# Kernel optimization log

Measured on AMD Instinct MI355X. Metric: run time of the kernel, lower is better.

The kernel has to match this reference:

```python
import jax, jax.numpy as jnp
import numpy as np

B, C, N = 16, 256, 2048
DA = C // 4
BN_EPS = 1e-5


def setup_inputs() -> dict:
    key = jax.random.key(0)
    ks = jax.random.split(key, 7)
    s = lambda fan_in: 1.0 / np.sqrt(fan_in)
    return {
        "x": jax.random.normal(ks[0], (B, C, N), dtype=jnp.float32),
        "Wq": jax.random.normal(ks[1], (DA, C), dtype=jnp.float32) * s(C),
        "Wk": jax.random.normal(ks[2], (DA, C), dtype=jnp.float32) * s(C),
        "Wv": jax.random.normal(ks[3], (C, C), dtype=jnp.float32) * s(C),
        "Wp": jax.random.normal(ks[4], (C, C), dtype=jnp.float32) * s(C),
        "gamma": jnp.ones((C,), dtype=jnp.float32),
        "beta": jnp.zeros((C,), dtype=jnp.float32),
    }


def reference(x, Wq, Wk, Wv, Wp, gamma, beta):
    # 1x1 conv projections (pointwise over N)
    q = jnp.einsum("dc,bcn->bnd", Wq, x)          # [B, N, da]
    k = jnp.einsum("dc,bcm->bdm", Wk, x)          # [B, da, N]
    v = jnp.einsum("oc,bcm->bmo", Wv, x)          # [B, N, C]

    energy = jnp.einsum("bnd,bdm->bnm", q, k)     # [B, N, N]
    # offset-attention double normalization: softmax over query axis (dim=1),
    # then L1 renormalization over key axis (dim=-1)
    attn = jax.nn.softmax(energy, axis=1)
    attn = attn / (1e-9 + attn.sum(axis=-1, keepdims=True))

    fsa = jnp.einsum("bnm,bmo->bon", attn, v)     # [B, C, N]

    # proj: Conv1d(1x1, no bias) -> BatchNorm1d (training-mode batch stats) -> ReLU
    y = x - fsa
    h = jnp.einsum("oc,bcn->bon", Wp, y)          # [B, C, N]
    mean = h.mean(axis=(0, 2), keepdims=True)
    var = h.var(axis=(0, 2), keepdims=True)       # biased variance
    h = (h - mean) * jax.lax.rsqrt(var + BN_EPS)
    h = h * gamma[None, :, None] + beta[None, :, None]
    h = jax.nn.relu(h)
    return h + x
```

## Files before the change

kernel.cpp:

```cpp
#include <hip/hip_runtime.h>
#include <math.h>

#define B_ 16
#define C_ 256
#define N_ 2048
#define D_ 64
#define NP_ 2080

typedef __attribute__((ext_vector_type(8))) short bf8;
typedef __attribute__((ext_vector_type(4))) float f4;

#define MFMA16(A, Bv, Cv) __builtin_amdgcn_mfma_f32_16x16x32_bf16(A, Bv, Cv, 0, 0, 0)

__device__ __forceinline__ short f2b(float f) {
  unsigned u = __float_as_uint(f);
  u = (u + 0x7fff + ((u >> 16) & 1)) >> 16;
  return (short)u;
}
__device__ __forceinline__ float b2f(short s) {
  return __uint_as_float(((unsigned)(unsigned short)s) << 16);
}

static constexpr size_t OFF_XT = 0;
static constexpr size_t OFF_QN = (size_t)16 << 20;
static constexpr size_t OFF_KN = (size_t)20 << 20;
static constexpr size_t OFF_VT = (size_t)24 << 20;
static constexpr size_t OFF_CI = (size_t)42 << 20;
static constexpr size_t OFF_WQ = OFF_CI + ((size_t)128 << 10);
static constexpr size_t OFF_WK = OFF_WQ + ((size_t)32 << 10);
static constexpr size_t OFF_WV = OFF_WK + ((size_t)32 << 10);
static constexpr size_t OFF_WP = OFF_WV + ((size_t)128 << 10);
static constexpr size_t OFF_S1 = OFF_WP + ((size_t)128 << 10);
static constexpr size_t OFF_S2 = OFF_S1 + 1024;
static constexpr size_t OFF_P1 = OFF_S2 + 4096;
static constexpr size_t OFF_P2 = OFF_P1 + ((size_t)512 << 10);

__global__ __launch_bounds__(256) void transpose_x_kernel(
    const float* __restrict__ x, short* __restrict__ xT,
    const float* __restrict__ fq, const float* __restrict__ fk,
    const float* __restrict__ fv, const float* __restrict__ fp,
    short* __restrict__ wq, short* __restrict__ wk,
    short* __restrict__ wv, short* __restrict__ wp) {
  if (blockIdx.z == 16) {
    int idx = (blockIdx.y * 32 + blockIdx.x) * 256 + threadIdx.x;
#pragma unroll
    for (int r = 0; r < 5; ++r) {
      int e = idx + r * 32768;
      if (e < 16384) wq[e] = f2b(fq[e]);
      else if (e < 32768) wk[e - 16384] = f2b(fk[e - 16384]);
      else if (e < 98304) wv[e - 32768] = f2b(fv[e - 32768]);
      else if (e < 163840) wp[e - 98304] = f2b(fp[e - 98304]);
    }
    return;
  }
  __shared__ float t[64][65];
  const int b = blockIdx.z, c0 = blockIdx.y * 64, n0 = blockIdx.x * 64;
  const int tid = threadIdx.x;
  const float* xp = x + ((size_t)b * C_ + c0) * N_ + n0;
#pragma unroll
  for (int i = 0; i < 16; ++i) {
    int idx = tid + i * 256;
    int cl = idx >> 6, nl = idx & 63;
    t[cl][nl] = xp[(size_t)cl * N_ + nl];
  }
  __syncthreads();
  short* op = xT + ((size_t)b * N_ + n0) * C_ + c0;
#pragma unroll
  for (int i = 0; i < 8; ++i) {
    int idx = tid + i * 256;
    int nl = idx >> 5, cl2 = (idx & 31) * 2;
    ushort2 v;
    v.x = (unsigned short)f2b(t[cl2][nl]);
    v.y = (unsigned short)f2b(t[cl2 + 1][nl]);
    *(ushort2*)(op + (size_t)nl * C_ + cl2) = v;
  }
}

__global__ __launch_bounds__(256, 4) void proj_qkv_kernel(
    const short* __restrict__ xT, const short* __restrict__ Wqb,
    const short* __restrict__ Wkb, const short* __restrict__ Wvb,
    short* __restrict__ Qn, short* __restrict__ Kn, short* __restrict__ Vt) {
  const int tid = threadIdx.x;
  const int wv = tid >> 6, lane = tid & 63;
  const int li = lane & 15, quad = lane >> 4;
  const int b = blockIdx.y, n0 = blockIdx.x * 64;
  const int n = n0 + wv * 16 + li;
  const short* xrow = xT + ((size_t)b * N_ + n) * C_ + quad * 8;
  if (blockIdx.z == 0) {
    f4 accq[4] = {}, acck[4] = {};
    for (int ks = 0; ks < 8; ++ks) {
      bf8 bfr = *(const bf8*)(xrow + ks * 32);
#pragma unroll
      for (int ot = 0; ot < 4; ++ot) {
        bf8 aq = *(const bf8*)(Wqb + (size_t)(ot * 16 + li) * C_ + ks * 32 + quad * 8);
        accq[ot] = MFMA16(aq, bfr, accq[ot]);
        bf8 ak = *(const bf8*)(Wkb + (size_t)(ot * 16 + li) * C_ + ks * 32 + quad * 8);
        acck[ot] = MFMA16(ak, bfr, acck[ot]);
      }
    }
#pragma unroll
    for (int ot = 0; ot < 4; ++ot) {
      short4 vq = {f2b(accq[ot].x), f2b(accq[ot].y), f2b(accq[ot].z), f2b(accq[ot].w)};
      *(short4*)(Qn + ((size_t)b * N_ + n) * D_ + ot * 16 + quad * 4) = vq;
      short4 vk = {f2b(acck[ot].x), f2b(acck[ot].y), f2b(acck[ot].z), f2b(acck[ot].w)};
      *(short4*)(Kn + ((size_t)b * N_ + n) * D_ + ot * 16 + quad * 4) = vk;
    }
  } else {
#pragma unroll
    for (int half = 0; half < 2; ++half) {
      f4 accv[2][4] = {};
      for (int ks = 0; ks < 8; ++ks) {
        bf8 bfr = *(const bf8*)(xrow + ks * 32);
#pragma unroll
        for (int vt = 0; vt < 2; ++vt)
#pragma unroll
          for (int ot = 0; ot < 4; ++ot) {
            bf8 av = *(const bf8*)(Wvb + (size_t)((half * 2 + vt) * 64 + ot * 16 + li) * C_ +
                                   ks * 32 + quad * 8);
            accv[vt][ot] = MFMA16(av, bfr, accv[vt][ot]);
          }
      }
#pragma unroll
      for (int vt = 0; vt < 2; ++vt)
#pragma unroll
        for (int ot = 0; ot < 4; ++ot)
#pragma unroll
          for (int r = 0; r < 4; ++r)
            Vt[((size_t)b * C_ + (half * 2 + vt) * 64 + ot * 16 + quad * 4 + r) * NP_ + n] =
                f2b(accv[vt][ot][r]);
    }
  }
}

__global__ __launch_bounds__(256, 2) void colstats_kernel(const short* __restrict__ Qn,
                                                          const short* __restrict__ Kn,
                                                          float* __restrict__ cinv) {
  __shared__ short qS[2][64][72];
  const int tid = threadIdx.x;
  const int wv = tid >> 6, lane = tid & 63;
  const int li = lane & 15, quad = lane >> 4;
  const int b = blockIdx.y, m0 = blockIdx.x * 64;
  const short* krow = Kn + ((size_t)b * N_ + m0 + wv * 16 + li) * D_ + quad * 8;
  bf8 af0 = *(const bf8*)(krow);
  bf8 af1 = *(const bf8*)(krow + 32);
  const short* Qb = Qn + (size_t)b * N_ * D_;
#pragma unroll
  for (int j = 0; j < 2; ++j) {
    int idx = tid * 2 + j;
    int row = idx >> 3, c8 = (idx & 7) * 8;
    *(bf8*)&qS[0][row][c8] = *(const bf8*)(Qb + (size_t)row * D_ + c8);
  }
  __syncthreads();
  float csum[4] = {0.f, 0.f, 0.f, 0.f};
  for (int t = 0; t < 32; ++t) {
    if (t < 31) {
#pragma unroll
      for (int j = 0; j < 2; ++j) {
        int idx = tid * 2 + j;
        int row = idx >> 3, c8 = (idx & 7) * 8;
        *(bf8*)&qS[(t + 1) & 1][row][c8] =
            *(const bf8*)(Qb + (size_t)((t + 1) * 64 + row) * D_ + c8);
      }
    }
#pragma unroll
    for (int nt = 0; nt < 4; ++nt) {
      bf8 b0 = *(const bf8*)&qS[t & 1][nt * 16 + li][quad * 8];
      bf8 b1 = *(const bf8*)&qS[t & 1][nt * 16 + li][32 + quad * 8];
      f4 s = {};
      s = MFMA16(af0, b0, s);
      s = MFMA16(af1, b1, s);
      csum[0] += __expf(s.x);
      csum[1] += __expf(s.y);
      csum[2] += __expf(s.z);
      csum[3] += __expf(s.w);
    }
    __syncthreads();
  }
#pragma unroll
  for (int r = 0; r < 4; ++r) {
#pragma unroll
    for (int m = 1; m < 16; m <<= 1) csum[r] += __shfl_xor(csum[r], m);
  }
  if (li == 0) {
#pragma unroll
    for (int r = 0; r < 4; ++r)
      cinv[(size_t)b * N_ + m0 + wv * 16 + quad * 4 + r] = 1.f / csum[r];
  }
}

__global__ __launch_bounds__(512, 2) void attn_fsa_kernel(
    const float* __restrict__ x, const short* __restrict__ Qn, const short* __restrict__ Kn,
    const short* __restrict__ Vt, const float* __restrict__ cinv, short* __restrict__ yT) {
  __shared__ short pT[2][64][136];
  __shared__ float civS[2048];
  __shared__ float racc[64];
  const int tid = threadIdx.x;
  const int wv = tid >> 6, lane = tid & 63;
  const int li = lane & 15, quad = lane >> 4;
  const int b = blockIdx.y, n0 = blockIdx.x * 64;
  *(float4*)(civS + tid * 4) = *(const float4*)(cinv + (size_t)b * N_ + tid * 4);
  if (tid < 64) racc[tid] = 0.f;
  bf8 q[4][2];
#pragma unroll
  for (int nt = 0; nt < 4; ++nt) {
    const short* qrow = Qn + ((size_t)b * N_ + n0 + nt * 16 + li) * D_ + quad * 8;
    q[nt][0] = *(const bf8*)(qrow);
    q[nt][1] = *(const bf8*)(qrow + 32);
  }
  __syncthreads();
  f4 acc[2][4] = {};
  float rloc[4] = {};
  const int ob = wv * 32;
  const short* Kb = Kn + (size_t)b * N_ * D_;
  const short* Vb = Vt + (size_t)b * C_ * NP_;
  {
    const short* krow = Kb + (size_t)(wv * 16 + li) * D_ + quad * 8;
    bf8 a0 = *(const bf8*)(krow);
    bf8 a1 = *(const bf8*)(krow + 32);
    f4 civ4 = *(const f4*)(civS + wv * 16 + quad * 4);
#pragma unroll
    for (int nt = 0; nt < 4; ++nt) {
      f4 s = {};
      s = MFMA16(a0, q[nt][0], s);
      s = MFMA16(a1, q[nt][1], s);
      short4 pv;
#pragma unroll
      for (int r = 0; r < 4; ++r) {
        float p = __expf(s[r]) * civ4[r];
        short ph = f2b(p);
        ((short*)&pv)[r] = ph;
        rloc[nt] += b2f(ph);
      }
      *(short4*)&pT[0][nt * 16 + li][wv * 16 + quad * 4] = pv;
    }
  }
  bf8 va[2][4];
#pragma unroll
  for (int ot = 0; ot < 2; ++ot)
#pragma unroll
    for (int kf = 0; kf < 4; ++kf)
      va[ot][kf] = *(const bf8*)(Vb + (size_t)(ob + ot * 16 + li) * NP_ + kf * 32 + quad * 8);
  __syncthreads();
  for (int t = 0; t < 16; ++t) {
    const int mm2 = (t + 1) * 128;
    bf8 vn[2][4], a0, a1;
    if (t < 15) {
#pragma unroll
      for (int ot = 0; ot < 2; ++ot)
#pragma unroll
        for (int kf = 0; kf < 4; ++kf)
          vn[ot][kf] = *(const bf8*)(Vb + (size_t)(ob + ot * 16 + li) * NP_ +
                                     mm2 + kf * 32 + quad * 8);
      const short* krow = Kb + (size_t)(mm2 + wv * 16 + li) * D_ + quad * 8;
      a0 = *(const bf8*)(krow);
      a1 = *(const bf8*)(krow + 32);
    }
    const short* Pb = &pT[t & 1][0][0];
#pragma unroll
    for (int nt = 0; nt < 4; ++nt) {
#pragma unroll
      for (int kf = 0; kf < 4; ++kf) {
        bf8 pb = *(const bf8*)(Pb + (size_t)(nt * 16 + li) * 136 + kf * 32 + quad * 8);
#pragma unroll
        for (int ot = 0; ot < 2; ++ot) acc[ot][nt] = MFMA16(va[ot][kf], pb, acc[ot][nt]);
      }
    }
    if (t < 15) {
      f4 civ4 = *(const f4*)(civS + mm2 + wv * 16 + quad * 4);
      short* Pw = &pT[(t + 1) & 1][0][0];
#pragma unroll
      for (int nt = 0; nt < 4; ++nt) {
        f4 s = {};
        s = MFMA16(a0, q[nt][0], s);
        s = MFMA16(a1, q[nt][1], s);
        short4 pv;
#pragma unroll
        for (int r = 0; r < 4; ++r) {
          float p = __expf(s[r]) * civ4[r];
          short ph = f2b(p);
          ((short*)&pv)[r] = ph;
          rloc[nt] += b2f(ph);
        }
        *(short4*)(Pw + (size_t)(nt * 16 + li) * 136 + wv * 16 + quad * 4) = pv;
      }
#pragma unroll
      for (int ot = 0; ot < 2; ++ot)
#pragma unroll
        for (int kf = 0; kf < 4; ++kf) va[ot][kf] = vn[ot][kf];
    }
    __syncthreads();
  }
#pragma unroll
  for (int nt = 0; nt < 4; ++nt) {
    float rv = rloc[nt];
    rv += __shfl_xor(rv, 16);
    rv += __shfl_xor(rv, 32);
    if (quad == 0) atomicAdd(&racc[nt * 16 + li], rv);
  }
  __syncthreads();
#pragma unroll
  for (int nt = 0; nt < 4; ++nt) {
    const int nn = n0 + nt * 16 + li;
    const float rinv = 1.f / (1e-9f + racc[nt * 16 + li]);
    short* yrow = yT + ((size_t)b * N_ + nn) * C_ + ob;
#pragma unroll
    for (int ot = 0; ot < 2; ++ot) {
      short4 v;
#pragma unroll
      for (int r = 0; r < 4; ++r) {
        int o = ob + ot * 16 + quad * 4 + r;
        float xv = x[((size_t)b * C_ + o) * N_ + nn];
        ((short*)&v)[r] = f2b(xv - acc[ot][nt][r] * rinv);
      }
      *(short4*)(yrow + ot * 16 + quad * 4) = v;
    }
  }
}

__global__ __launch_bounds__(256, 4) void wp_kernel(const short* __restrict__ yT,
                                                    const short* __restrict__ Wp,
                                                    float* __restrict__ H,
                                                    float* __restrict__ P1,
                                                    float* __restrict__ P2) {
  __shared__ alignas(16) float ha[64][68];
  __shared__ float red1[64][4];
  __shared__ float red2[64][4];
  const int tid = threadIdx.x;
  const int wv = tid >> 6, lane = tid & 63;
  const int li = lane & 15, quad = lane >> 4;
  const int b = blockIdx.y, n0 = blockIdx.x * 64, o0 = blockIdx.z * 64;
  const int n = n0 + wv * 16 + li;
  const short* yrow = yT + ((size_t)b * N_ + n) * C_ + quad * 8;
  f4 acc[4] = {};
  for (int ks = 0; ks < 8; ++ks) {
    bf8 bfr = *(const bf8*)(yrow + ks * 32);
#pragma unroll
    for (int ot = 0; ot < 4; ++ot) {
      bf8 afr = *(const bf8*)(Wp + (size_t)(o0 + ot * 16 + li) * C_ + ks * 32 + quad * 8);
      acc[ot] = MFMA16(afr, bfr, acc[ot]);
    }
  }
#pragma unroll
  for (int ot = 0; ot < 4; ++ot)
#pragma unroll
    for (int r = 0; r < 4; ++r) ha[ot * 16 + quad * 4 + r][wv * 16 + li] = acc[ot][r];
  __syncthreads();
  const int o = tid >> 2, nq = tid & 3;
  float s1p = 0.f, s2p = 0.f;
  float* hrow = H + ((size_t)b * C_ + o0 + o) * N_ + n0 + nq * 16;
#pragma unroll
  for (int j4 = 0; j4 < 4; ++j4) {
    float4 v = *reinterpret_cast<const float4*>(&ha[o][nq * 16 + j4 * 4]);
    s1p += v.x + v.y + v.z + v.w;
    s2p += v.x * v.x + v.y * v.y + v.z * v.z + v.w * v.w;
    reinterpret_cast<float4*>(hrow)[j4] = v;
  }
  red1[o][nq] = s1p;
  red2[o][nq] = s2p;
  __syncthreads();
  if (tid < 64) {
    float a1 = red1[tid][0] + red1[tid][1] + red1[tid][2] + red1[tid][3];
    float a2 = red2[tid][0] + red2[tid][1] + red2[tid][2] + red2[tid][3];
    const int g = b * 32 + blockIdx.x;
    P1[(size_t)g * 256 + o0 + tid] = a1;
    P2[(size_t)g * 256 + o0 + tid] = a2;
  }
}

__global__ __launch_bounds__(256) void bn_reduce_kernel(const float* __restrict__ P1,
                                                        const float* __restrict__ P2,
                                                        float* __restrict__ S1,
                                                        float* __restrict__ S2) {
  const int lc = threadIdx.x >> 4, gl = threadIdx.x & 15;
  const int c = blockIdx.x * 16 + lc;
  float a1 = 0.f, a2 = 0.f;
#pragma unroll
  for (int k = 0; k < 32; ++k) {
    int g = gl + k * 16;
    a1 += P1[(size_t)g * 256 + c];
    a2 += P2[(size_t)g * 256 + c];
  }
#pragma unroll
  for (int m = 1; m < 16; m <<= 1) {
    a1 += __shfl_xor(a1, m);
    a2 += __shfl_xor(a2, m);
  }
  if (gl == 0) {
    S1[c] = a1;
    S2[c] = a2;
  }
}

__global__ __launch_bounds__(256) void bn_apply_kernel(const float* __restrict__ H,
                                                       const float* __restrict__ x,
                                                       const float* __restrict__ S1,
                                                       const float* __restrict__ S2,
                                                       const float* __restrict__ gamma,
                                                       const float* __restrict__ beta,
                                                       float* __restrict__ out) {
  size_t idx = ((size_t)blockIdx.x * 256 + threadIdx.x) * 4;
  int o = (int)((idx >> 11) & 255);
  const float invn = 1.f / ((float)B_ * N_);
  float mean = S1[o] * invn;
  float var = S2[o] * invn - mean * mean;
  float inv = rsqrtf(var + 1e-5f);
  float a = gamma[o] * inv;
  float c = beta[o] - mean * a;
  float4 h = *reinterpret_cast<const float4*>(&H[idx]);
  float4 xv = *reinterpret_cast<const float4*>(&x[idx]);
  float4 r;
  r.x = fmaxf(h.x * a + c, 0.f) + xv.x;
  r.y = fmaxf(h.y * a + c, 0.f) + xv.y;
  r.z = fmaxf(h.z * a + c, 0.f) + xv.z;
  r.w = fmaxf(h.w * a + c, 0.f) + xv.w;
  *reinterpret_cast<float4*>(&out[idx]) = r;
}

extern "C" void kernel_launch(void* const* d_in, const int* in_sizes, int n_in,
                              void* d_out, int out_size, void* d_ws, size_t ws_size,
                              hipStream_t stream) {
  (void)in_sizes; (void)n_in; (void)out_size; (void)ws_size;
  const float* x = (const float*)d_in[0];
  const float* Wq = (const float*)d_in[1];
  const float* Wk = (const float*)d_in[2];
  const float* Wv = (const float*)d_in[3];
  const float* Wp = (const float*)d_in[4];
  const float* gamma = (const float*)d_in[5];
  const float* beta = (const float*)d_in[6];
  char* ws = (char*)d_ws;
  short* xT = (short*)(ws + OFF_XT);
  short* Qn = (short*)(ws + OFF_QN);
  short* Kn = (short*)(ws + OFF_KN);
  short* Vt = (short*)(ws + OFF_VT);
  float* CI = (float*)(ws + OFF_CI);
  short* Wqb = (short*)(ws + OFF_WQ);
  short* Wkb = (short*)(ws + OFF_WK);
  short* Wvb = (short*)(ws + OFF_WV);
  short* Wpb = (short*)(ws + OFF_WP);
  float* S1 = (float*)(ws + OFF_S1);
  float* S2 = (float*)(ws + OFF_S2);
  float* P1 = (float*)(ws + OFF_P1);
  float* P2 = (float*)(ws + OFF_P2);
  short* yT = xT;
  float* out = (float*)d_out;
  float* H = out;

  dim3 blk(256);
  transpose_x_kernel<<<dim3(32, 4, 17), blk, 0, stream>>>(x, xT, Wq, Wk, Wv, Wp,
                                                          Wqb, Wkb, Wvb, Wpb);
  proj_qkv_kernel<<<dim3(32, 16, 2), blk, 0, stream>>>(xT, Wqb, Wkb, Wvb, Qn, Kn, Vt);
  colstats_kernel<<<dim3(32, 16), blk, 0, stream>>>(Qn, Kn, CI);
  attn_fsa_kernel<<<dim3(32, 16), dim3(512), 0, stream>>>(x, Qn, Kn, Vt, CI, yT);
  wp_kernel<<<dim3(32, 16, 4), blk, 0, stream>>>(yT, Wpb, H, P1, P2);
  bn_reduce_kernel<<<dim3(16), blk, 0, stream>>>(P1, P2, S1, S2);
  bn_apply_kernel<<<dim3(8192), blk, 0, stream>>>(H, x, S1, S2, gamma, beta, out);
}
```

Measured before the change: 304.5 us.

## Recompute Wp GEMM in BN apply pass instead of materializing H

```diff
diff --git a/kernel.cpp b/kernel.cpp
--- a/kernel.cpp
+++ b/kernel.cpp
@@ -319,7 +319,6 @@
 
 __global__ __launch_bounds__(256, 4) void wp_kernel(const short* __restrict__ yT,
                                                     const short* __restrict__ Wp,
-                                                    float* __restrict__ H,
                                                     float* __restrict__ P1,
                                                     float* __restrict__ P2) {
   __shared__ alignas(16) float ha[64][68];
@@ -347,13 +346,11 @@
   __syncthreads();
   const int o = tid >> 2, nq = tid & 3;
   float s1p = 0.f, s2p = 0.f;
-  float* hrow = H + ((size_t)b * C_ + o0 + o) * N_ + n0 + nq * 16;
 #pragma unroll
   for (int j4 = 0; j4 < 4; ++j4) {
     float4 v = *reinterpret_cast<const float4*>(&ha[o][nq * 16 + j4 * 4]);
     s1p += v.x + v.y + v.z + v.w;
     s2p += v.x * v.x + v.y * v.y + v.z * v.z + v.w * v.w;
-    reinterpret_cast<float4*>(hrow)[j4] = v;
   }
   red1[o][nq] = s1p;
   red2[o][nq] = s2p;
@@ -391,29 +388,61 @@
   }
 }
 
-__global__ __launch_bounds__(256) void bn_apply_kernel(const float* __restrict__ H,
-                                                       const float* __restrict__ x,
-                                                       const float* __restrict__ S1,
-                                                       const float* __restrict__ S2,
-                                                       const float* __restrict__ gamma,
-                                                       const float* __restrict__ beta,
-                                                       float* __restrict__ out) {
-  size_t idx = ((size_t)blockIdx.x * 256 + threadIdx.x) * 4;
-  int o = (int)((idx >> 11) & 255);
-  const float invn = 1.f / ((float)B_ * N_);
-  float mean = S1[o] * invn;
-  float var = S2[o] * invn - mean * mean;
-  float inv = rsqrtf(var + 1e-5f);
-  float a = gamma[o] * inv;
-  float c = beta[o] - mean * a;
-  float4 h = *reinterpret_cast<const float4*>(&H[idx]);
-  float4 xv = *reinterpret_cast<const float4*>(&x[idx]);
-  float4 r;
-  r.x = fmaxf(h.x * a + c, 0.f) + xv.x;
-  r.y = fmaxf(h.y * a + c, 0.f) + xv.y;
-  r.z = fmaxf(h.z * a + c, 0.f) + xv.z;
-  r.w = fmaxf(h.w * a + c, 0.f) + xv.w;
-  *reinterpret_cast<float4*>(&out[idx]) = r;
+__global__ __launch_bounds__(256, 2) void bn_apply_gemm_kernel(
+    const short* __restrict__ yT, const short* __restrict__ Wp,
+    const float* __restrict__ S1, const float* __restrict__ S2,
+    const float* __restrict__ gamma, const float* __restrict__ beta,
+    const float* __restrict__ x, float* __restrict__ out) {
+  __shared__ alignas(16) float ha[64][68];
+  __shared__ float abA[256], abC[256];
+  const int tid = threadIdx.x;
+  const int wv = tid >> 6, lane = tid & 63;
+  const int li = lane & 15, quad = lane >> 4;
+  const int b = blockIdx.y, n0 = blockIdx.x * 64;
+  {
+    const float invn = 1.f / ((float)B_ * N_);
+    float mean = S1[tid] * invn;
+    float var = S2[tid] * invn - mean * mean;
+    float a = gamma[tid] * rsqrtf(var + 1e-5f);
+    abA[tid] = a;
+    abC[tid] = beta[tid] - mean * a;
+  }
+  const int n = n0 + wv * 16 + li;
+  const short* yrow = yT + ((size_t)b * N_ + n) * C_ + quad * 8;
+  bf8 yr[8];
+#pragma unroll
+  for (int ks = 0; ks < 8; ++ks) yr[ks] = *(const bf8*)(yrow + ks * 32);
+  const int o = tid >> 2, nq = tid & 3;
+  for (int o0 = 0; o0 < 256; o0 += 64) {
+    f4 acc[4] = {};
+#pragma unroll
+    for (int ks = 0; ks < 8; ++ks)
+#pragma unroll
+      for (int ot = 0; ot < 4; ++ot) {
+        bf8 afr = *(const bf8*)(Wp + (size_t)(o0 + ot * 16 + li) * C_ + ks * 32 + quad * 8);
+        acc[ot] = MFMA16(afr, yr[ks], acc[ot]);
+      }
+    __syncthreads();
+#pragma unroll
+    for (int ot = 0; ot < 4; ++ot)
+#pragma unroll
+      for (int r = 0; r < 4; ++r) ha[ot * 16 + quad * 4 + r][wv * 16 + li] = acc[ot][r];
+    __syncthreads();
+    const float a = abA[o0 + o], c = abC[o0 + o];
+    const float* xrow = x + ((size_t)b * C_ + o0 + o) * N_ + n0 + nq * 16;
+    float* orow = out + ((size_t)b * C_ + o0 + o) * N_ + n0 + nq * 16;
+#pragma unroll
+    for (int j4 = 0; j4 < 4; ++j4) {
+      float4 v = *reinterpret_cast<const float4*>(&ha[o][nq * 16 + j4 * 4]);
+      float4 xv = reinterpret_cast<const float4*>(xrow)[j4];
+      float4 rr;
+      rr.x = fmaxf(v.x * a + c, 0.f) + xv.x;
+      rr.y = fmaxf(v.y * a + c, 0.f) + xv.y;
+      rr.z = fmaxf(v.z * a + c, 0.f) + xv.z;
+      rr.w = fmaxf(v.w * a + c, 0.f) + xv.w;
+      reinterpret_cast<float4*>(orow)[j4] = rr;
+    }
+  }
 }
 
 extern "C" void kernel_launch(void* const* d_in, const int* in_sizes, int n_in,
@@ -443,7 +472,6 @@
   float* P2 = (float*)(ws + OFF_P2);
   short* yT = xT;
   float* out = (float*)d_out;
-  float* H = out;
 
   dim3 blk(256);
   transpose_x_kernel<<<dim3(32, 4, 17), blk, 0, stream>>>(x, xT, Wq, Wk, Wv, Wp,
@@ -451,7 +479,8 @@
   proj_qkv_kernel<<<dim3(32, 16, 2), blk, 0, stream>>>(xT, Wqb, Wkb, Wvb, Qn, Kn, Vt);
   colstats_kernel<<<dim3(32, 16), blk, 0, stream>>>(Qn, Kn, CI);
   attn_fsa_kernel<<<dim3(32, 16), dim3(512), 0, stream>>>(x, Qn, Kn, Vt, CI, yT);
-  wp_kernel<<<dim3(32, 16, 4), blk, 0, stream>>>(yT, Wpb, H, P1, P2);
+  wp_kernel<<<dim3(32, 16, 4), blk, 0, stream>>>(yT, Wpb, P1, P2);
   bn_reduce_kernel<<<dim3(16), blk, 0, stream>>>(P1, P2, S1, S2);
-  bn_apply_kernel<<<dim3(8192), blk, 0, stream>>>(H, x, S1, S2, gamma, beta, out);
-}
+  bn_apply_gemm_kernel<<<dim3(32, 16), blk, 0, stream>>>(yT, Wpb, S1, S2, gamma, beta,
+                                                         x, out);
+}
```

After: 323.8 us. +6.3%, slower.
